# Kernel tuning notes

Measured on AMD Instinct MI355X. Metric: run time of the kernel, lower is better.

Reference implementation:

```python
import jax, jax.numpy as jnp
import numpy as np

B, L, D = 4, 2048, 1024
NUM_HEADS = 1
HEAD_DIM = D // NUM_HEADS  # 1024


def setup_inputs() -> dict:
    key = jax.random.key(0)
    ks = jax.random.split(key, 12)
    s = 1.0 / np.sqrt(D)
    return {
        "query": jax.random.normal(ks[0], (B, L, D), jnp.float32),
        "key": jax.random.normal(ks[1], (B, L, D), jnp.float32),
        "value": jax.random.normal(ks[2], (B, L, D), jnp.float32),
        "mask": jax.random.randint(ks[3], (B, 1, L, L), 0, 2, jnp.int32),
        "Wq": jax.random.uniform(ks[4], (D, D * NUM_HEADS), jnp.float32, -s, s),
        "bq": jnp.zeros((D * NUM_HEADS,), jnp.float32),
        "Wk": jax.random.uniform(ks[5], (D, D * NUM_HEADS), jnp.float32, -s, s),
        "bk": jnp.zeros((D * NUM_HEADS,), jnp.float32),
        "Wv": jax.random.uniform(ks[6], (D, D * NUM_HEADS), jnp.float32, -s, s),
        "bv": jnp.zeros((D * NUM_HEADS,), jnp.float32),
        "Wo": jax.random.uniform(ks[7], (D * NUM_HEADS, D), jnp.float32, -s, s),
        "bo": jnp.zeros((D,), jnp.float32),
    }


def reference(query, key, value, mask, Wq, bq, Wk, bk, Wv, bv, Wo, bo):
    b, lq = query.shape[0], query.shape[1]
    lk = key.shape[1]
    # project and split heads: (B, L, H, Dh) -> (B, H, L, Dh)
    Q = (query @ Wq + bq).reshape(b, lq, NUM_HEADS, HEAD_DIM).transpose(0, 2, 1, 3)
    K = (key @ Wk + bk).reshape(b, lk, NUM_HEADS, HEAD_DIM).transpose(0, 2, 1, 3)
    V = (value @ Wv + bv).reshape(b, lk, NUM_HEADS, HEAD_DIM).transpose(0, 2, 1, 3)
    scale = 1.0 / jnp.sqrt(jnp.float32(HEAD_DIM))
    scores = jnp.einsum("bhqd,bhkd->bhqk", Q, K) * scale  # (B,H,Lq,Lk)
    scores = jnp.where(mask == 0, jnp.float32(-1e20), scores)
    attn = jax.nn.softmax(scores, axis=-1)
    out = jnp.einsum("bhqk,bhkd->bhqd", attn, V)  # (B,H,Lq,Dh)
    out = out.transpose(0, 2, 1, 3).reshape(b, lq, NUM_HEADS * HEAD_DIM)
    return out @ Wo + bo
```

## Files before the change

kernel.cpp:

```cpp
#include <hip/hip_runtime.h>

#define B_ 4
#define L_ 2048
#define D_ 1024
#define M_FLAT (B_*L_)
#define NE_ ((size_t)M_FLAT * D_)
#define WE_ ((size_t)D_ * D_)

typedef unsigned short bf16_t;
typedef __attribute__((ext_vector_type(8))) short bf16x8;
typedef __attribute__((ext_vector_type(4))) float f32x4;

__device__ __forceinline__ bf16_t f2bf(float f) {
  union { float f; unsigned int u; } c; c.f = f;
  unsigned int u = c.u;
  unsigned int r = (u + 0x7fffu + ((u >> 16) & 1u)) >> 16;
  return (bf16_t)r;
}
__device__ __forceinline__ float bf2f(bf16_t h) {
  union { unsigned int u; float f; } c; c.u = ((unsigned int)h) << 16;
  return c.f;
}

__device__ __forceinline__ void gload_lds16(const bf16_t* g, bf16_t* l) {
  __builtin_amdgcn_global_load_lds(
      (const __attribute__((address_space(1))) unsigned int*)g,
      (__attribute__((address_space(3))) unsigned int*)l, 16, 0, 0);
}

#define BARRIER() do { asm volatile("" ::: "memory"); \
                       __builtin_amdgcn_s_barrier();  \
                       asm volatile("" ::: "memory"); } while (0)

__global__ __launch_bounds__(256) void prep_all(
    const float* __restrict__ q, const float* __restrict__ k,
    const float* __restrict__ v, const int* __restrict__ mask,
    const float* __restrict__ Wq, const float* __restrict__ Wk,
    const float* __restrict__ Wo, const float* __restrict__ Wv,
    const float* __restrict__ bv,
    bf16_t* __restrict__ outbase,
    bf16_t* __restrict__ xq,
    unsigned long long* __restrict__ bm,
    float* __restrict__ c2part) {
  __shared__ float t[32][33];
  const int b = blockIdx.x, tid = threadIdx.x;
  if (b < 12288) {
    const float* in; bf16_t* out; size_t li;
    if (b < 4096)      { in = q; out = xq;           li = (size_t)b * 256 + tid; }
    else if (b < 8192) { in = k; out = xq + NE_;     li = (size_t)(b - 4096) * 256 + tid; }
    else               { in = v; out = xq + 2 * NE_; li = (size_t)(b - 8192) * 256 + tid; }
    const float4* p = (const float4*)in + li * 2;
    float4 a = p[0], bb = p[1];
    union { bf16_t h[8]; uint4 u; } r;
    r.h[0] = f2bf(a.x); r.h[1] = f2bf(a.y); r.h[2] = f2bf(a.z); r.h[3] = f2bf(a.w);
    r.h[4] = f2bf(bb.x); r.h[5] = f2bf(bb.y); r.h[6] = f2bf(bb.z); r.h[7] = f2bf(bb.w);
    ((uint4*)out)[li] = r.u;
  } else if (b < 28672) {
    size_t base = (size_t)(b - 12288) * 1024;
    size_t wb = base + (size_t)(tid >> 6) * 256;
    int lane = tid & 63;
    int m0 = mask[wb + lane];
    int m1 = mask[wb + 64 + lane];
    int m2 = mask[wb + 128 + lane];
    int m3 = mask[wb + 192 + lane];
    unsigned long long b0 = __ballot(m0 != 0);
    unsigned long long b1 = __ballot(m1 != 0);
    unsigned long long b2 = __ballot(m2 != 0);
    unsigned long long b3 = __ballot(m3 != 0);
    if (lane == 0) {
      size_t wo = wb >> 6;
      bm[wo] = b0; bm[wo + 1] = b1; bm[wo + 2] = b2; bm[wo + 3] = b3;
    }
  } else if (b < 32768) {
    int bb = b - 28672;
    int zz = bb >> 10, rem = bb & 1023;
    int bx = rem & 31, by = rem >> 5;
    int tx = tid & 31, ty = tid >> 5;
    int c0 = bx * 32, r0 = by * 32;
    if (zz == 3) {
      bf16_t* o = outbase + 4 * WE_;
#pragma unroll
      for (int i = 0; i < 4; i++) {
        size_t idx = (size_t)(r0 + ty + i * 8) * D_ + c0 + tx;
        o[idx] = f2bf(Wv[idx]);
      }
      return;
    }
    const float* Wsrc = (zz == 0) ? Wq : (zz == 1) ? Wk : Wo;
    bf16_t* Wt = outbase + (size_t)(zz == 2 ? 3 : zz) * WE_;
#pragma unroll
    for (int i = 0; i < 4; i++)
      t[ty + i * 8][tx] = Wsrc[(size_t)(r0 + ty + i * 8) * D_ + c0 + tx];
    __syncthreads();
#pragma unroll
    for (int i = 0; i < 4; i++)
      Wt[(size_t)(c0 + ty + i * 8) * D_ + r0 + tx] = f2bf(t[tx][ty + i * 8]);
  } else {
    int bb = b - 32768;
    int kc = bb >> 2, jb = bb & 3;
    int j = jb * 256 + tid;
    const float* wp = Wo + (size_t)(kc * 128) * D_ + j;
    const float* bp = bv + kc * 128;
    float s = 0.f;
#pragma unroll 8
    for (int kk = 0; kk < 128; kk++) s += bp[kk] * wp[(size_t)kk * D_];
    c2part[kc * D_ + j] = s;
  }
}

__global__ __launch_bounds__(256) void w2_reduce(const float* __restrict__ pw,
                                                 bf16_t* __restrict__ w2t,
                                                 const float* __restrict__ c2part,
                                                 float* __restrict__ c2) {
  __shared__ float t[32][33];
  int c0 = blockIdx.x * 32, r0 = blockIdx.y * 32;
  int tx = threadIdx.x, ty = threadIdx.y;
#pragma unroll
  for (int i = 0; i < 4; i++) {
    size_t idx = (size_t)(r0 + ty + i * 8) * D_ + c0 + tx;
    float s = 0.f;
#pragma unroll
    for (int zz = 0; zz < 8; zz++) s += pw[(size_t)zz * WE_ + idx];
    t[ty + i * 8][tx] = s;
  }
  __syncthreads();
#pragma unroll
  for (int i = 0; i < 4; i++)
    w2t[(size_t)(c0 + ty + i * 8) * D_ + r0 + tx] = f2bf(t[tx][ty + i * 8]);
  if (blockIdx.y == 0 && ty == 0) {
    int c = c0 + tx;
    float s = 0.f;
#pragma unroll
    for (int kc = 0; kc < 8; kc++) s += c2part[kc * D_ + c];
    c2[c] = s;
  }
}

#define MODE_PROJ 0
#define MODE_S    1
#define MODE_FIN  2
#define MODE_TRK  3

template <int BM, int MODE>
__global__ __launch_bounds__(512, 2)
void g8(const bf16_t* __restrict__ Abase, int lda, long strA,
        const bf16_t* __restrict__ Bbase, int ldb, long strB,
        void* __restrict__ outp, long strO, int ldo,
        const float* __restrict__ x0, const float* __restrict__ x1,
        const float* __restrict__ x2,
        const void* __restrict__ auxp, float* __restrict__ rsp,
        int K) {
  constexpr int WROWS = BM / 2;
  constexpr int QAF   = WROWS / 32;
  constexpr int MFR   = WROWS / 16;
  constexpr int AL    = BM / 128;
  constexpr int BL    = 2;
  constexpr int AHB   = WROWS * 128;
  constexpr int BUFB  = (BM + 256) * 128;
  extern __shared__ __align__(16) char smem[];

  const int tid = threadIdx.x, lane = tid & 63, w = tid >> 6;
  const int wm = w >> 2, wn = w & 3;
  const int fr = lane & 15, fs = lane >> 4;
  const int z = blockIdx.z;

  int gx = gridDim.x, nxy = gx * gridDim.y;
  int lin = blockIdx.y * gx + blockIdx.x;
  if ((nxy & 7) == 0) { int q = nxy >> 3; lin = (lin & 7) * q + (lin >> 3); }
  const int xb = lin % gx;
  const int mbase = (lin / gx) * BM, nbase = xb * 256;

  const bf16_t* A  = Abase + (size_t)z * strA;
  const bf16_t* Bt = Bbase + (size_t)z * strB;

  int offA[2][2], offB[2][2];
#pragma unroll
  for (int h = 0; h < 2; h++)
#pragma unroll
    for (int i = 0; i < 2; i++) {
      int c = i * 512 + tid, row = c >> 3;
      int sg = (c & 7) ^ (row & 7);
      if (i < AL) offA[h][i] = (mbase + h * WROWS + row) * lda + sg * 8;
      offB[h][i] = (nbase + h * 128 + row) * ldb + sg * 8;
    }

  const int swz0 = (fs ^ (fr & 7)) * 16;
  const int swz1 = ((4 + fs) ^ (fr & 7)) * 16;

  bf16x8 af[QAF][2], bfv[2][2][2];
  f32x4 acc[MFR][4] = {};

#define STAGE_A(h, kt, bsel) do {                                             \
    char* hb_ = smem + (bsel) * BUFB + (h) * AHB;                             \
    _Pragma("unroll")                                                         \
    for (int i_ = 0; i_ < AL; ++i_)                                           \
      gload_lds16(A + offA[h][i_] + (kt) * 64,                                \
                  (bf16_t*)(hb_ + (i_ * 512 + tid) * 16));                    \
  } while (0)
#define STAGE_B(h, kt, bsel) do {                                             \
    char* hb_ = smem + (bsel) * BUFB + BM * 128 + (h) * 16384;                \
    _Pragma("unroll")                                                         \
    for (int i_ = 0; i_ < BL; ++i_)                                           \
      gload_lds16(Bt + offB[h][i_] + (kt) * 64,                               \
                  (bf16_t*)(hb_ + (i_ * 512 + tid) * 16));                    \
  } while (0)
#define LOAD_A(bsel, mh) do {                                                 \
    const char* ab_ = smem + (bsel) * BUFB + (wm * WROWS) * 128;              \
    _Pragma("unroll")                                                         \
    for (int i_ = 0; i_ < QAF; ++i_) {                                        \
      int rb_ = ((mh) * (WROWS / 2) + i_ * 16 + fr) * 128;                    \
      af[i_][0] = *(const bf16x8*)(ab_ + rb_ + swz0);                         \
      af[i_][1] = *(const bf16x8*)(ab_ + rb_ + swz1);                         \
    }                                                                         \
  } while (0)
#define LOAD_B(bsel, nh) do {                                                 \
    const char* bb_ = smem + (bsel) * BUFB + BM * 128 + (wn * 64) * 128;      \
    _Pragma("unroll")                                                         \
    for (int j_ = 0; j_ < 2; ++j_) {                                          \
      int rb_ = ((nh) * 32 + j_ * 16 + fr) * 128;                             \
      bfv[nh][j_][0] = *(const bf16x8*)(bb_ + rb_ + swz0);                    \
      bfv[nh][j_][1] = *(const bf16x8*)(bb_ + rb_ + swz1);                    \
    }                                                                         \
  } while (0)
#define MFMA_Q(mh, nh) do {                                                   \
    __builtin_amdgcn_s_setprio(1);                                            \
    _Pragma("unroll")                                                         \
    for (int i_ = 0; i_ < QAF; ++i_)                                          \
    _Pragma("unroll")                                                         \
    for (int j_ = 0; j_ < 2; ++j_) {                                          \
      acc[(mh)*QAF + i_][(nh)*2 + j_] = __builtin_amdgcn_mfma_f32_16x16x32_bf16( \
          af[i_][0], bfv[nh][j_][0], acc[(mh)*QAF + i_][(nh)*2 + j_], 0, 0, 0);  \
      acc[(mh)*QAF + i_][(nh)*2 + j_] = __builtin_amdgcn_mfma_f32_16x16x32_bf16( \
          af[i_][1], bfv[nh][j_][1], acc[(mh)*QAF + i_][(nh)*2 + j_], 0, 0, 0);  \
    }                                                                         \
    __builtin_amdgcn_s_setprio(0);                                            \
  } while (0)
#define VMWN() do {                                                           \
    if constexpr (AL == 2) asm volatile("s_waitcnt vmcnt(8)" ::: "memory");   \
    else                   asm volatile("s_waitcnt vmcnt(6)" ::: "memory");   \
  } while (0)
#define LGKM0() asm volatile("s_waitcnt lgkmcnt(0)" ::: "memory")

  const int NK = K >> 6, NI = NK >> 1;

  if constexpr (MODE == MODE_FIN) {
    float* rl = (float*)(smem + 2 * BUFB);
    int rrow = tid >> 2, rq = tid & 3;
    const float* rp = x0 + ((size_t)z * L_ + mbase + rrow) * 32 + rq * 8;
    float s_ = 0.f;
#pragma unroll
    for (int j_ = 0; j_ < 8; ++j_) s_ += rp[j_];
    rl[rrow * 4 + rq] = s_;
    LGKM0();
  }

  STAGE_B(0, 0, 0); STAGE_B(1, 0, 0); STAGE_A(0, 0, 0); STAGE_A(1, 0, 0);
  STAGE_B(0, 1, 1); STAGE_B(1, 1, 1); STAGE_A(0, 1, 1); STAGE_A(1, 1, 1);
  VMWN(); BARRIER();

  for (int it = 0; it < NI; ++it) {
    const int ta = (2 * it + 2 < NK) ? 2 * it + 2 : NK - 1;
    const int tb = (2 * it + 3 < NK) ? 2 * it + 3 : NK - 1;
    LOAD_A(0, 0); LOAD_B(0, 0); MFMA_Q(0, 0);
    LOAD_B(0, 1);               MFMA_Q(0, 1);
    LOAD_A(0, 1);               MFMA_Q(1, 1);
                                MFMA_Q(1, 0);
    BARRIER();
    STAGE_B(0, ta, 0); STAGE_B(1, ta, 0); STAGE_A(0, ta, 0); STAGE_A(1, ta, 0);
    VMWN();
    BARRIER();
    LOAD_A(1, 0); LOAD_B(1, 0); MFMA_Q(0, 0);
    LOAD_B(1, 1);               MFMA_Q(0, 1);
    LOAD_A(1, 1);               MFMA_Q(1, 1);
                                MFMA_Q(1, 0);
    BARRIER();
    STAGE_B(0, tb, 1); STAGE_B(1, tb, 1); STAGE_A(0, tb, 1); STAGE_A(1, tb, 1);
    VMWN();
    BARRIER();
  }
  asm volatile("s_waitcnt vmcnt(0)" ::: "memory");

  const int r0 = mbase + wm * WROWS;
  const int c0 = nbase + wn * 64;

  if constexpr (MODE == MODE_PROJ) {
    BARRIER();
    char* ep = smem + w * AHB;
    if (z < 2) {
      bf16_t* o = (bf16_t*)outp + (size_t)z * strO;
      const float* bias = (z == 0) ? x0 : x1;
      const float scale = (z == 0) ? 0.03125f : 1.0f;
#pragma unroll
      for (int nf = 0; nf < 4; ++nf) {
        float bv = bias[c0 + nf * 16 + fr];
#pragma unroll
        for (int mf = 0; mf < MFR; ++mf)
#pragma unroll
          for (int jj = 0; jj < 4; ++jj) {
            int row = mf * 16 + fs * 4 + jj;
            int slot = (nf * 2 + (fr >> 3)) ^ ((row >> 1) & 7);
            *(bf16_t*)(ep + row * 128 + slot * 16 + (fr & 7) * 2) =
                f2bf((acc[mf][nf][jj] + bv) * scale);
          }
      }
      LGKM0();
      const int rl = lane >> 3, sl = lane & 7;
#pragma unroll
      for (int i = 0; i < WROWS / 8; ++i) {
        int row = i * 8 + rl;
        int slot = sl ^ ((row >> 1) & 7);
        uint4 vv = *(const uint4*)(ep + row * 128 + slot * 16);
        *(uint4*)&o[(size_t)(r0 + row) * ldo + c0 + sl * 8] = vv;
      }
    } else {
      bf16_t* ob = (bf16_t*)auxp;
      const int bidx = r0 >> 11, rb = r0 & (L_ - 1);
      ob += (size_t)bidx * D_ * L_;
#pragma unroll
      for (int nf = 0; nf < 4; ++nf) {
        int coll = nf * 16 + fr;
        float bv = x2[c0 + coll];
        int xm = (coll & (WROWS / 8 - 1)) << 3;
#pragma unroll
        for (int mf = 0; mf < MFR; ++mf) {
          int rbase = mf * 16 + fs * 4;
          union { bf16_t h[4]; uint2 u; } pk;
#pragma unroll
          for (int jj = 0; jj < 4; ++jj) pk.h[jj] = f2bf(acc[mf][nf][jj] + bv);
          *(uint2*)(ep + coll * (WROWS * 2) + 2 * (rbase ^ xm)) = pk.u;
        }
      }
      LGKM0();
      constexpr int LPC = WROWS / 8;
      constexpr int CPI = 64 / LPC;
      const int colr = lane / LPC;
      const int rc = (lane % LPC) * 8;
#pragma unroll
      for (int i2 = 0; i2 < LPC; ++i2) {
        int coll = i2 * CPI + colr;
        int xm = (coll & (WROWS / 8 - 1)) << 3;
        uint4 vv = *(const uint4*)(ep + coll * (WROWS * 2) + 2 * (rc ^ xm));
        *(uint4*)&ob[(size_t)(c0 + coll) * L_ + rb + rc] = vv;
      }
    }
  } else if constexpr (MODE == MODE_TRK) {
    float* o = (float*)outp + (size_t)z * strO;
#pragma unroll
    for (int mf = 0; mf < MFR; ++mf) {
#pragma unroll
      for (int jj = 0; jj < 4; ++jj) {
        int r = r0 + mf * 16 + fs * 4 + jj;
#pragma unroll
        for (int nf = 0; nf < 4; ++nf)
          o[(size_t)r * ldo + c0 + nf * 16 + fr] = acc[mf][nf][jj];
      }
    }
  } else if constexpr (MODE == MODE_S) {
    BARRIER();
    char* ep = smem + w * AHB;
    bf16_t* o = (bf16_t*)outp + (size_t)z * strO;
    const unsigned long long* bw =
        (const unsigned long long*)auxp +
        ((size_t)z * L_ + r0) * 32 + (c0 >> 6);
#pragma unroll
    for (int mf = 0; mf < MFR; ++mf) {
#pragma unroll
      for (int jj = 0; jj < 4; ++jj) {
        int row = mf * 16 + fs * 4 + jj;
        unsigned long long wd = bw[(size_t)row * 32];
        float psum = 0.f;
#pragma unroll
        for (int nf = 0; nf < 4; ++nf) {
          int cbit = nf * 16 + fr;
          float e = ((wd >> cbit) & 1ull) ? __expf(acc[mf][nf][jj]) : 0.0f;
          bf16_t eb = f2bf(e);
          psum += bf2f(eb);
          int slot = (nf * 2 + (fr >> 3)) ^ ((row >> 1) & 7);
          *(bf16_t*)(ep + row * 128 + slot * 16 + (fr & 7) * 2) = eb;
        }
#pragma unroll
        for (int off = 8; off; off >>= 1) psum += __shfl_xor(psum, off, 16);
        if (fr == 0)
          rsp[((size_t)z * L_ + r0 + row) * 32 + xb * 4 + wn] = psum;
      }
    }
    LGKM0();
    const int rl = lane >> 3, sl = lane & 7;
#pragma unroll
    for (int i = 0; i < WROWS / 8; ++i) {
      int row = i * 8 + rl;
      int slot = sl ^ ((row >> 1) & 7);
      uint4 vv = *(const uint4*)(ep + row * 128 + slot * 16);
      *(uint4*)&o[(size_t)(r0 + row) * ldo + c0 + sl * 8] = vv;
    }
  } else {
    float* o = (float*)outp + (size_t)z * strO;
    const float* rl = (const float*)(smem + 2 * BUFB);
#pragma unroll
    for (int mf = 0; mf < MFR; ++mf) {
#pragma unroll
      for (int jj = 0; jj < 4; ++jj) {
        int r = r0 + mf * 16 + fs * 4 + jj;
        int rloc = wm * WROWS + mf * 16 + fs * 4 + jj;
        float rsv = rl[rloc * 4] + rl[rloc * 4 + 1] +
                    rl[rloc * 4 + 2] + rl[rloc * 4 + 3];
        float inv = 1.0f / fmaxf(rsv, 1e-30f);
#pragma unroll
        for (int nf = 0; nf < 4; ++nf) {
          int c = c0 + nf * 16 + fr;
          o[(size_t)r * ldo + c] = acc[mf][nf][jj] * inv + x1[c];
        }
      }
    }
  }
#undef STAGE_A
#undef STAGE_B
#undef LOAD_A
#undef LOAD_B
#undef MFMA_Q
#undef VMWN
#undef LGKM0
}

extern "C" void kernel_launch(void* const* d_in, const int* in_sizes, int n_in,
                              void* d_out, int out_size, void* d_ws, size_t ws_size,
                              hipStream_t stream) {
  const float* query = (const float*)d_in[0];
  const float* keyi  = (const float*)d_in[1];
  const float* value = (const float*)d_in[2];
  const int*   mask  = (const int*)d_in[3];
  const float* Wq = (const float*)d_in[4];
  const float* bq = (const float*)d_in[5];
  const float* Wk = (const float*)d_in[6];
  const float* bk = (const float*)d_in[7];
  const float* Wv = (const float*)d_in[8];
  const float* bv = (const float*)d_in[9];
  const float* Wo = (const float*)d_in[10];
  const float* bo = (const float*)d_in[11];

  bf16_t* ws = (bf16_t*)d_ws;
  bf16_t* XQ   = ws;
  bf16_t* XK   = ws + NE_;
  bf16_t* XV   = ws + 2 * NE_;
  bf16_t* WQT  = ws + 3 * NE_;
  bf16_t* WKT  = WQT + WE_;
  bf16_t* W2T  = WKT + WE_;
  bf16_t* WOT  = W2T + WE_;
  bf16_t* WVb  = WOT + WE_;
  bf16_t* Qb   = WVb + WE_;
  bf16_t* Kb   = Qb + NE_;
  bf16_t* VWt  = Kb + NE_;
  float*  c2p  = (float*)(VWt + NE_);
  float*  rspart = c2p + D_;
  unsigned long long* bmask =
      (unsigned long long*)(rspart + (size_t)B_ * L_ * 32);
  float*  c2part = (float*)(bmask + (size_t)B_ * L_ * L_ / 64);
  bf16_t* Sb   = ws;
  float*  pW2  = (float*)Qb;

  hipFuncSetAttribute((const void*)g8<128, MODE_PROJ>,
                      hipFuncAttributeMaxDynamicSharedMemorySize, 98304);
  hipFuncSetAttribute((const void*)g8<256, MODE_S>,
                      hipFuncAttributeMaxDynamicSharedMemorySize, 131072);
  hipFuncSetAttribute((const void*)g8<128, MODE_TRK>,
                      hipFuncAttributeMaxDynamicSharedMemorySize, 98304);
  hipFuncSetAttribute((const void*)g8<128, MODE_FIN>,
                      hipFuncAttributeMaxDynamicSharedMemorySize, 100352);

  prep_all<<<dim3(32800), dim3(256), 0, stream>>>(
      query, keyi, value, mask, Wq, Wk, Wo, Wv, bv, WQT, XQ, bmask, c2part);
  g8<128, MODE_TRK><<<dim3(4, 8, 8), 512, 98304, stream>>>(
      WVb, D_, 128, WOT, D_, 128, pW2, (long)WE_, D_,
      nullptr, nullptr, nullptr, nullptr, nullptr, 128);
  w2_reduce<<<dim3(32, 32), dim3(32, 8), 0, stream>>>(pW2, W2T, c2part, c2p);
  g8<128, MODE_PROJ><<<dim3(4, 64, 3), 512, 98304, stream>>>(
      XQ, D_, (long)NE_, WQT, D_, (long)WE_, Qb, (long)NE_, D_,
      bq, bk, c2p, VWt, nullptr, D_);
  g8<256, MODE_S><<<dim3(8, 8, 4), 512, 131072, stream>>>(
      Qb, D_, (long)L_ * D_, Kb, D_, (long)L_ * D_, Sb, (long)L_ * L_, L_,
      nullptr, nullptr, nullptr, bmask, rspart, D_);
  g8<128, MODE_FIN><<<dim3(4, 16, 4), 512, 100352, stream>>>(
      Sb, L_, (long)L_ * L_, VWt, L_, (long)D_ * L_, d_out, (long)L_ * D_, D_,
      rspart, bo, nullptr, nullptr, nullptr, L_);
}
```

Measured before the change: 216.9 us.

## Single-buffer projection GEMM to cut LDS and raise occupancy

For the projection GEMM mode only, the double-buffered LDS pipeline becomes a single buffer with a full vmcnt(0) wait each K step. The epilogue is split into two halves so each wave needs only 4 KB of staging. Together these halve dynamic shared memory to 48 KB, and launch bounds rise to 6 blocks per CU so more blocks can hide latency. The cost is lost prefetch overlap inside each block and tighter register limits that may cause spilling.

```diff
diff --git a/kernel.cpp b/kernel.cpp
--- a/kernel.cpp
+++ b/kernel.cpp
@@ -142,7 +142,7 @@
 #define MODE_TRK  3
 
 template <int BM, int MODE>
-__global__ __launch_bounds__(512, 2)
+__global__ __launch_bounds__(512, (MODE == MODE_PROJ) ? 6 : 2)
 void g8(const bf16_t* __restrict__ Abase, int lda, long strA,
         const bf16_t* __restrict__ Bbase, int ldb, long strB,
         void* __restrict__ outp, long strO, int ldo,
@@ -150,6 +150,7 @@
         const float* __restrict__ x2,
         const void* __restrict__ auxp, float* __restrict__ rsp,
         int K) {
+  constexpr bool SB = (MODE == MODE_PROJ);
   constexpr int WROWS = BM / 2;
   constexpr int QAF   = WROWS / 32;
   constexpr int MFR   = WROWS / 16;
@@ -239,6 +240,7 @@
     if constexpr (AL == 2) asm volatile("s_waitcnt vmcnt(8)" ::: "memory");   \
     else                   asm volatile("s_waitcnt vmcnt(6)" ::: "memory");   \
   } while (0)
+#define VMW0() asm volatile("s_waitcnt vmcnt(0)" ::: "memory")
 #define LGKM0() asm volatile("s_waitcnt lgkmcnt(0)" ::: "memory")
 
   const int NK = K >> 6, NI = NK >> 1;
@@ -254,93 +256,123 @@
     LGKM0();
   }
 
-  STAGE_B(0, 0, 0); STAGE_B(1, 0, 0); STAGE_A(0, 0, 0); STAGE_A(1, 0, 0);
-  STAGE_B(0, 1, 1); STAGE_B(1, 1, 1); STAGE_A(0, 1, 1); STAGE_A(1, 1, 1);
-  VMWN(); BARRIER();
-
-  for (int it = 0; it < NI; ++it) {
-    const int ta = (2 * it + 2 < NK) ? 2 * it + 2 : NK - 1;
-    const int tb = (2 * it + 3 < NK) ? 2 * it + 3 : NK - 1;
-    LOAD_A(0, 0); LOAD_B(0, 0); MFMA_Q(0, 0);
-    LOAD_B(0, 1);               MFMA_Q(0, 1);
-    LOAD_A(0, 1);               MFMA_Q(1, 1);
-                                MFMA_Q(1, 0);
-    BARRIER();
-    STAGE_B(0, ta, 0); STAGE_B(1, ta, 0); STAGE_A(0, ta, 0); STAGE_A(1, ta, 0);
-    VMWN();
-    BARRIER();
-    LOAD_A(1, 0); LOAD_B(1, 0); MFMA_Q(0, 0);
-    LOAD_B(1, 1);               MFMA_Q(0, 1);
-    LOAD_A(1, 1);               MFMA_Q(1, 1);
-                                MFMA_Q(1, 0);
-    BARRIER();
-    STAGE_B(0, tb, 1); STAGE_B(1, tb, 1); STAGE_A(0, tb, 1); STAGE_A(1, tb, 1);
-    VMWN();
-    BARRIER();
+  if constexpr (SB) {
+    STAGE_B(0, 0, 0); STAGE_B(1, 0, 0); STAGE_A(0, 0, 0); STAGE_A(1, 0, 0);
+    VMW0(); BARRIER();
+    for (int t = 0; t < NK; ++t) {
+      LOAD_A(0, 0); LOAD_B(0, 0); MFMA_Q(0, 0);
+      LOAD_B(0, 1);               MFMA_Q(0, 1);
+      LOAD_A(0, 1);               MFMA_Q(1, 1);
+                                  MFMA_Q(1, 0);
+      BARRIER();
+      if (t + 1 < NK) {
+        STAGE_B(0, t + 1, 0); STAGE_B(1, t + 1, 0);
+        STAGE_A(0, t + 1, 0); STAGE_A(1, t + 1, 0);
+        VMW0();
+      }
+      BARRIER();
+    }
+  } else {
+    STAGE_B(0, 0, 0); STAGE_B(1, 0, 0); STAGE_A(0, 0, 0); STAGE_A(1, 0, 0);
+    STAGE_B(0, 1, 1); STAGE_B(1, 1, 1); STAGE_A(0, 1, 1); STAGE_A(1, 1, 1);
+    VMWN(); BARRIER();
+    for (int it = 0; it < NI; ++it) {
+      const int ta = (2 * it + 2 < NK) ? 2 * it + 2 : NK - 1;
+      const int tb = (2 * it + 3 < NK) ? 2 * it + 3 : NK - 1;
+      LOAD_A(0, 0); LOAD_B(0, 0); MFMA_Q(0, 0);
+      LOAD_B(0, 1);               MFMA_Q(0, 1);
+      LOAD_A(0, 1);               MFMA_Q(1, 1);
+                                  MFMA_Q(1, 0);
+      BARRIER();
+      STAGE_B(0, ta, 0); STAGE_B(1, ta, 0); STAGE_A(0, ta, 0); STAGE_A(1, ta, 0);
+      VMWN();
+      BARRIER();
+      LOAD_A(1, 0); LOAD_B(1, 0); MFMA_Q(0, 0);
+      LOAD_B(1, 1);               MFMA_Q(0, 1);
+      LOAD_A(1, 1);               MFMA_Q(1, 1);
+                                  MFMA_Q(1, 0);
+      BARRIER();
+      STAGE_B(0, tb, 1); STAGE_B(1, tb, 1); STAGE_A(0, tb, 1); STAGE_A(1, tb, 1);
+      VMWN();
+      BARRIER();
+    }
+    VMW0();
   }
-  asm volatile("s_waitcnt vmcnt(0)" ::: "memory");
 
   const int r0 = mbase + wm * WROWS;
   const int c0 = nbase + wn * 64;
 
   if constexpr (MODE == MODE_PROJ) {
     BARRIER();
-    char* ep = smem + w * AHB;
+    char* ep = smem + w * 4096;
     if (z < 2) {
       bf16_t* o = (bf16_t*)outp + (size_t)z * strO;
       const float* bias = (z == 0) ? x0 : x1;
       const float scale = (z == 0) ? 0.03125f : 1.0f;
 #pragma unroll
-      for (int nf = 0; nf < 4; ++nf) {
-        float bv = bias[c0 + nf * 16 + fr];
-#pragma unroll
-        for (int mf = 0; mf < MFR; ++mf)
-#pragma unroll
-          for (int jj = 0; jj < 4; ++jj) {
-            int row = mf * 16 + fs * 4 + jj;
-            int slot = (nf * 2 + (fr >> 3)) ^ ((row >> 1) & 7);
-            *(bf16_t*)(ep + row * 128 + slot * 16 + (fr & 7) * 2) =
-                f2bf((acc[mf][nf][jj] + bv) * scale);
+      for (int p = 0; p < 2; ++p) {
+#pragma unroll
+        for (int nf = 0; nf < 4; ++nf) {
+          float bv = bias[c0 + nf * 16 + fr];
+#pragma unroll
+          for (int mfl = 0; mfl < 2; ++mfl) {
+            int mf = p * 2 + mfl;
+#pragma unroll
+            for (int jj = 0; jj < 4; ++jj) {
+              int row = mf * 16 + fs * 4 + jj;
+              int rloc = row - p * 32;
+              int slot = (nf * 2 + (fr >> 3)) ^ ((row >> 1) & 7);
+              *(bf16_t*)(ep + rloc * 128 + slot * 16 + (fr & 7) * 2) =
+                  f2bf((acc[mf][nf][jj] + bv) * scale);
+            }
           }
-      }
-      LGKM0();
-      const int rl = lane >> 3, sl = lane & 7;
-#pragma unroll
-      for (int i = 0; i < WROWS / 8; ++i) {
-        int row = i * 8 + rl;
-        int slot = sl ^ ((row >> 1) & 7);
-        uint4 vv = *(const uint4*)(ep + row * 128 + slot * 16);
-        *(uint4*)&o[(size_t)(r0 + row) * ldo + c0 + sl * 8] = vv;
+        }
+        LGKM0();
+        const int rl2 = lane >> 3, sl = lane & 7;
+#pragma unroll
+        for (int i = 0; i < 4; ++i) {
+          int row = p * 32 + i * 8 + rl2;
+          int rloc = row - p * 32;
+          int slot = sl ^ ((row >> 1) & 7);
+          uint4 vv = *(const uint4*)(ep + rloc * 128 + slot * 16);
+          *(uint4*)&o[(size_t)(r0 + row) * ldo + c0 + sl * 8] = vv;
+        }
+        LGKM0();
       }
     } else {
       bf16_t* ob = (bf16_t*)auxp;
       const int bidx = r0 >> 11, rb = r0 & (L_ - 1);
       ob += (size_t)bidx * D_ * L_;
 #pragma unroll
-      for (int nf = 0; nf < 4; ++nf) {
-        int coll = nf * 16 + fr;
-        float bv = x2[c0 + coll];
-        int xm = (coll & (WROWS / 8 - 1)) << 3;
-#pragma unroll
-        for (int mf = 0; mf < MFR; ++mf) {
-          int rbase = mf * 16 + fs * 4;
-          union { bf16_t h[4]; uint2 u; } pk;
-#pragma unroll
-          for (int jj = 0; jj < 4; ++jj) pk.h[jj] = f2bf(acc[mf][nf][jj] + bv);
-          *(uint2*)(ep + coll * (WROWS * 2) + 2 * (rbase ^ xm)) = pk.u;
+      for (int p = 0; p < 2; ++p) {
+#pragma unroll
+        for (int nfl = 0; nfl < 2; ++nfl) {
+          int nf = p * 2 + nfl;
+          int coll = nf * 16 + fr;
+          int cloc = coll - p * 32;
+          float bv = x2[c0 + coll];
+          int xm = (coll & 7) << 3;
+#pragma unroll
+          for (int mf = 0; mf < MFR; ++mf) {
+            int rbase = mf * 16 + fs * 4;
+            union { bf16_t h[4]; uint2 u; } pk;
+#pragma unroll
+            for (int jj = 0; jj < 4; ++jj) pk.h[jj] = f2bf(acc[mf][nf][jj] + bv);
+            *(uint2*)(ep + cloc * 128 + 2 * (rbase ^ xm)) = pk.u;
+          }
         }
-      }
-      LGKM0();
-      constexpr int LPC = WROWS / 8;
-      constexpr int CPI = 64 / LPC;
-      const int colr = lane / LPC;
-      const int rc = (lane % LPC) * 8;
-#pragma unroll
-      for (int i2 = 0; i2 < LPC; ++i2) {
-        int coll = i2 * CPI + colr;
-        int xm = (coll & (WROWS / 8 - 1)) << 3;
-        uint4 vv = *(const uint4*)(ep + coll * (WROWS * 2) + 2 * (rc ^ xm));
-        *(uint4*)&ob[(size_t)(c0 + coll) * L_ + rb + rc] = vv;
+        LGKM0();
+        const int colr = lane >> 3;
+        const int rc = (lane & 7) * 8;
+#pragma unroll
+        for (int i2 = 0; i2 < 4; ++i2) {
+          int coll = p * 32 + i2 * 8 + colr;
+          int cloc = coll - p * 32;
+          int xm = (coll & 7) << 3;
+          uint4 vv = *(const uint4*)(ep + cloc * 128 + 2 * (rc ^ xm));
+          *(uint4*)&ob[(size_t)(c0 + coll) * L_ + rb + rc] = vv;
+        }
+        LGKM0();
       }
     }
   } else if constexpr (MODE == MODE_TRK) {
@@ -419,6 +451,7 @@
 #undef LOAD_B
 #undef MFMA_Q
 #undef VMWN
+#undef VMW0
 #undef LGKM0
 }
 
@@ -459,7 +492,7 @@
   float*  pW2  = (float*)Qb;
 
   hipFuncSetAttribute((const void*)g8<128, MODE_PROJ>,
-                      hipFuncAttributeMaxDynamicSharedMemorySize, 98304);
+                      hipFuncAttributeMaxDynamicSharedMemorySize, 49152);
   hipFuncSetAttribute((const void*)g8<256, MODE_S>,
                       hipFuncAttributeMaxDynamicSharedMemorySize, 131072);
   hipFuncSetAttribute((const void*)g8<128, MODE_TRK>,
@@ -473,7 +506,7 @@
       WVb, D_, 128, WOT, D_, 128, pW2, (long)WE_, D_,
       nullptr, nullptr, nullptr, nullptr, nullptr, 128);
   w2_reduce<<<dim3(32, 32), dim3(32, 8), 0, stream>>>(pW2, W2T, c2part, c2p);
-  g8<128, MODE_PROJ><<<dim3(4, 64, 3), 512, 98304, stream>>>(
+  g8<128, MODE_PROJ><<<dim3(4, 64, 3), 512, 49152, stream>>>(
       XQ, D_, (long)NE_, WQT, D_, (long)WE_, Qb, (long)NE_, D_,
       bq, bk, c2p, VWt, nullptr, D_);
   g8<256, MODE_S><<<dim3(8, 8, 4), 512, 131072, stream>>>(
```

After: 625.8 us. 188% more time.
